# Kernel optimization log

Hardware: AMD Instinct MI355X
Metric: run time of the kernel (lower is better)

Reference implementation:

```python
import jax, jax.numpy as jnp
import numpy as np

HIDDEN = 1024
HEADS = 16
HEAD_DIM = HIDDEN // HEADS
B, T = 4, 2048


def setup_inputs() -> dict:
    key = jax.random.key(0)
    k_x, k_w1, k_b1, k_w2, k_b2 = jax.random.split(key, 5)
    lim1 = 1.0 / np.sqrt(HIDDEN)
    x = jax.random.normal(k_x, (B, T, HIDDEN), dtype=jnp.float32)
    # causal lower-triangular mask, broadcastable to [B, H, T, T]
    mask = jnp.tril(jnp.ones((T, T), dtype=jnp.int32))[None, None, :, :]
    # qkv_proj: Linear(HIDDEN, 3*HIDDEN); torch Linear: y = x @ W.T + b
    W_qkv = jax.random.uniform(k_w1, (3 * HIDDEN, HIDDEN), minval=-lim1, maxval=lim1, dtype=jnp.float32)
    b_qkv = jax.random.uniform(k_b1, (3 * HIDDEN,), minval=-lim1, maxval=lim1, dtype=jnp.float32)
    W_out = jax.random.uniform(k_w2, (HIDDEN, HIDDEN), minval=-lim1, maxval=lim1, dtype=jnp.float32)
    b_out = jax.random.uniform(k_b2, (HIDDEN,), minval=-lim1, maxval=lim1, dtype=jnp.float32)
    return {"x": x, "mask": mask, "W_qkv": W_qkv, "b_qkv": b_qkv, "W_out": W_out, "b_out": b_out}


def reference(x, mask, W_qkv, b_qkv, W_out, b_out):
    Bx, Tx, C = x.shape
    qkv = x @ W_qkv.T + b_qkv                      # [B, T, 3C]
    qkv = qkv.reshape(Bx, Tx, 3, HEADS, HEAD_DIM)
    qkv = jnp.transpose(qkv, (2, 0, 3, 1, 4))      # [3, B, H, T, Dh]
    Q, K, V = qkv[0], qkv[1], qkv[2]
    scale = 1.0 / np.sqrt(HEAD_DIM)
    scores = jnp.einsum('bhqd,bhkd->bhqk', Q, K) * scale  # [B, H, T, T]
    scores = jnp.where(mask == 0, -jnp.inf, scores)
    probs = jax.nn.softmax(scores, axis=-1)
    ctx = jnp.einsum('bhqk,bhkd->bhqd', probs, V)  # [B, H, T, Dh]
    ctx = jnp.transpose(ctx, (0, 2, 1, 3)).reshape(Bx, Tx, C)
    return ctx @ W_out.T + b_out
```

## Files before the change

### kernel.cpp

```cpp
#include <hip/hip_runtime.h>
#include <cstdint>
#include <cstddef>

#define B_ 4
#define T_ 2048
#define C_ 1024
#define H_ 16
#define D_ 64

typedef __attribute__((ext_vector_type(8))) __bf16 bf16x8;
typedef __attribute__((ext_vector_type(4))) float floatx4;

#define QSCL (0.125f * 1.44269504088896f)
#define FMAX 24.0f

__device__ __forceinline__ unsigned short f2bf(float f) {
  union { float f; unsigned int u; } v; v.f = f;
  unsigned int r = v.u + 0x7fffu + ((v.u >> 16) & 1u);
  return (unsigned short)(r >> 16);
}
__device__ __forceinline__ ushort4 pk4(float a, float b, float c, float d) {
  ushort4 u; u.x = f2bf(a); u.y = f2bf(b); u.z = f2bf(c); u.w = f2bf(d);
  return u;
}
__device__ __forceinline__ bf16x8 cvt8(float4 a, float4 b) {
  bf16x8 r;
  r[0] = a.x; r[1] = a.y; r[2] = a.z; r[3] = a.w;
  r[4] = b.x; r[5] = b.y; r[6] = b.z; r[7] = b.w;
  return r;
}
__device__ __forceinline__ ushort4 pk4c(float a, float b, float c, float d) {
  union { __bf16 b4[4]; ushort4 u; } w;
  w.b4[0] = (__bf16)a; w.b4[1] = (__bf16)b; w.b4[2] = (__bf16)c; w.b4[3] = (__bf16)d;
  return w.u;
}

__device__ __forceinline__ void gl_lds16(const void* g, void* l) {
  __builtin_amdgcn_global_load_lds(
      (const __attribute__((address_space(1))) unsigned int*)g,
      (__attribute__((address_space(3))) unsigned int*)l, 16, 0, 0);
}

__global__ __launch_bounds__(256)
void conv_bf16(const float* __restrict__ src, unsigned short* __restrict__ dst,
               int n8) {
  for (int i = blockIdx.x * 256 + threadIdx.x; i < n8; i += gridDim.x * 256) {
    const float4* s = (const float4*)src + 2 * (size_t)i;
    float4 a = s[0], b = s[1];
    ((bf16x8*)dst)[i] = cvt8(a, b);
  }
}

template<int EPI, int GATHER, int WBF>
__global__ __launch_bounds__(256, 3)
void gemm_bt(const unsigned short* __restrict__ Abf,
             const void* __restrict__ Wraw,
             const float* __restrict__ bias,
             float* __restrict__ out,
             unsigned short* __restrict__ qws,
             unsigned short* __restrict__ kws,
             unsigned short* __restrict__ vtws)
{
  alignas(16) __shared__ unsigned short As[128 * 64];
  alignas(16) __shared__ unsigned short Bs[WBF ? 128 * 64 : 128 * 72];
  const int tid  = threadIdx.x;
  const int lane = tid & 63;
  const int wid  = tid >> 6;
  const int col  = lane & 15;
  const int quad = lane >> 4;
  const int wm = (wid >> 1) << 6;
  const int wn = (wid & 1) << 6;
  const int bm = blockIdx.y << 7;
  const int bn = blockIdx.x << 7;

  const float* Wf          = (const float*)Wraw;
  const unsigned short* Wb = (const unsigned short*)Wraw;

  const int r0 = tid >> 3;
  const int c0 = tid & 7;

  floatx4 acc[4][4];
#pragma unroll
  for (int i = 0; i < 4; ++i)
#pragma unroll
    for (int j = 0; j < 4; ++j)
      acc[i][j] = (floatx4){0.f, 0.f, 0.f, 0.f};

  for (int k0 = 0; k0 < 1024; k0 += 64) {
    __syncthreads();
#pragma unroll
    for (int s = 0; s < 4; ++s) {
      const int row  = (s << 5) + r0;
      const int colE = ((c0 ^ (row & 7)) << 3);
      const unsigned short* gsrc;
      if (GATHER) {
        const int m = bm + row;
        const int b = m >> 11, t = m & 2047;
        const int h = k0 >> 6;
        gsrc = Abf + ((((size_t)(b * 16 + h) << 11) + t) << 6) + colE;
      } else {
        gsrc = Abf + (size_t)(bm + row) * 1024 + k0 + colE;
      }
      gl_lds16(gsrc, (char*)As + (s << 12) + (wid << 10));
    }
    if (WBF) {
#pragma unroll
      for (int s = 0; s < 4; ++s) {
        const int row  = (s << 5) + r0;
        const int colE = ((c0 ^ (row & 7)) << 3);
        const unsigned short* gsrc = Wb + (size_t)(bn + row) * 1024 + k0 + colE;
        gl_lds16(gsrc, (char*)Bs + (s << 12) + (wid << 10));
      }
    } else {
#pragma unroll
      for (int s = 0; s < 4; ++s) {
        const int row = (s << 5) + r0;
        const int kc  = c0 << 3;
        const float* wsrc = &Wf[(size_t)(bn + row) * 1024 + k0 + kc];
        float4 w0 = *(const float4*)wsrc;
        float4 w1 = *(const float4*)(wsrc + 4);
        *(bf16x8*)&Bs[row * 72 + kc] = cvt8(w0, w1);
      }
    }
    __syncthreads();
#pragma unroll
    for (int kk = 0; kk < 64; kk += 32) {
      bf16x8 af[4], bfr[4];
#pragma unroll
      for (int i = 0; i < 4; ++i) {
        const int r = wm + i * 16 + col;
        af[i] = *(const bf16x8*)&As[(r << 6) + ((kk + quad * 8) ^ ((r & 7) << 3))];
      }
#pragma unroll
      for (int j = 0; j < 4; ++j) {
        const int r = wn + j * 16 + col;
        if (WBF)
          bfr[j] = *(const bf16x8*)&Bs[(r << 6) + ((kk + quad * 8) ^ ((r & 7) << 3))];
        else
          bfr[j] = *(const bf16x8*)&Bs[r * 72 + kk + quad * 8];
      }
#pragma unroll
      for (int i = 0; i < 4; ++i)
#pragma unroll
        for (int j = 0; j < 4; ++j)
          acc[i][j] = __builtin_amdgcn_mfma_f32_16x16x32_bf16(af[i], bfr[j], acc[i][j], 0, 0, 0);
    }
  }

#pragma unroll
  for (int i = 0; i < 4; ++i) {
    const int row = bm + wm + i * 16 + quad * 4;
#pragma unroll
    for (int j = 0; j < 4; ++j) {
      const int n  = bn + wn + j * 16 + col;
      const float bv = bias[n];
      float v[4];
#pragma unroll
      for (int r = 0; r < 4; ++r) v[r] = acc[i][j][r] + bv;

      if (EPI == 1) {
#pragma unroll
        for (int r = 0; r < 4; ++r)
          out[(size_t)(row + r) * 1024 + n] = v[r];
      } else {
        const int s   = n >> 10;
        const int rem = n & 1023;
        const int h   = rem >> 6;
        const int d   = rem & 63;
        const int b   = row >> 11;
        const int t   = row & 2047;
        const size_t bh = (size_t)(b * H_ + h);
        if (s == 0) {
#pragma unroll
          for (int r = 0; r < 4; ++r)
            qws[(bh * T_ + t + r) * D_ + d] = f2bf(v[r] * QSCL);
        } else if (s == 1) {
#pragma unroll
          for (int r = 0; r < 4; ++r)
            kws[(bh * T_ + t + r) * D_ + d] = f2bf(v[r]);
        } else {
          *(ushort4*)&vtws[(bh * D_ + d) * T_ + t] = pk4(v[0], v[1], v[2], v[3]);
        }
      }
    }
  }
}

__global__ __launch_bounds__(256, 2)
void attn_causal(unsigned short* __restrict__ qws,
                 const unsigned short* __restrict__ kws,
                 const unsigned short* __restrict__ vtws)
{
  alignas(16) __shared__ unsigned short Ks[2][64 * 64];
  alignas(16) __shared__ unsigned short Vs[2][64 * 64];
  alignas(16) __shared__ unsigned short Ps[4][2][16][72];
  const int tid  = threadIdx.x;
  const int lane = tid & 63;
  const int wid  = tid >> 6;
  const int col  = lane & 15;
  const int quad = lane >> 4;

  const int bh = blockIdx.x & 63;
  const int pr = blockIdx.x >> 6;

  const unsigned short* Kp  = kws + (size_t)bh * T_ * D_;
  const unsigned short* Vtp = vtws + (size_t)bh * D_ * T_;

  const int srow8 = lane >> 3;
  const int swz   = ((lane & 7) ^ srow8) << 3;

#define STAGE(kt_, b_)                                                        \
  do {                                                                        \
    _Pragma("unroll") for (int c2 = 0; c2 < 2; ++c2) {                        \
      const int cb = wid + (c2 << 2);                   \
      gl_lds16(Kp + ((size_t)(((kt_) << 6) + (cb << 3) + srow8) << 6) + swz,  \
               (char*)&Ks[b_][0] + (cb << 10));                               \
      gl_lds16(Vtp + ((size_t)((cb << 3) + srow8) << 11) + ((kt_) << 6) + swz,\
               (char*)&Vs[b_][0] + (cb << 10));                               \
    }                                                                         \
  } while (0)

#pragma unroll
  for (int half = 0; half < 2; ++half) {
    const int band = (half == 0) ? pr : (15 - pr);
    const int nk   = (band << 1) + 2;
    const int q0   = (band << 7) + (wid << 5);
    unsigned short* Qp = qws + ((size_t)bh * T_ + q0) * D_;

    bf16x8 bq[2][2];
#pragma unroll
    for (int h = 0; h < 2; ++h) {
      bq[h][0] = *(const bf16x8*)&Qp[(h * 16 + col) * D_ + quad * 8];
      bq[h][1] = *(const bf16x8*)&Qp[(h * 16 + col) * D_ + 32 + quad * 8];
    }

    floatx4 o[2][4];
#pragma unroll
    for (int h = 0; h < 2; ++h)
#pragma unroll
      for (int j = 0; j < 4; ++j) o[h][j] = (floatx4){0.f, 0.f, 0.f, 0.f};
    float lrow[2] = {0.f, 0.f};

    STAGE(0, 0);
    __syncthreads();

    for (int kt = 0; kt < nk; ++kt) {
      const int buf = kt & 1;
      if (kt + 1 < nk) STAGE(kt + 1, buf ^ 1);

      const unsigned short* Kb = &Ks[buf][0];
      bf16x8 kA[4], kB[4];
#pragma unroll
      for (int g = 0; g < 4; ++g) {
        const int r = g * 16 + col;
        kA[g] = *(const bf16x8*)&Kb[(r << 6) + ((quad ^ (col & 7)) << 3)];
        kB[g] = *(const bf16x8*)&Kb[(r << 6) + (((quad | 4) ^ (col & 7)) << 3)];
      }

      floatx4 s[2][4];
#pragma unroll
      for (int h = 0; h < 2; ++h)
#pragma unroll
        for (int g = 0; g < 4; ++g) {
          s[h][g] = (floatx4){0.f, 0.f, 0.f, 0.f};
          s[h][g] = __builtin_amdgcn_mfma_f32_16x16x32_bf16(kA[g], bq[h][0], s[h][g], 0, 0, 0);
          s[h][g] = __builtin_amdgcn_mfma_f32_16x16x32_bf16(kB[g], bq[h][1], s[h][g], 0, 0, 0);
        }

      if (kt >= nk - 2) {
#pragma unroll
        for (int h = 0; h < 2; ++h) {
          const int lim = q0 - (kt << 6) + (h << 4) + col;
#pragma unroll
          for (int g = 0; g < 4; ++g)
#pragma unroll
            for (int r = 0; r < 4; ++r)
              if (g * 16 + quad * 4 + r > lim) s[h][g][r] = -1e30f;
        }
      }

#pragma unroll
      for (int h = 0; h < 2; ++h) {
#pragma unroll
        for (int g = 0; g < 4; ++g)
#pragma unroll
          for (int r = 0; r < 4; ++r)
            s[h][g][r] = exp2f(s[h][g][r] - FMAX);
        lrow[h] += ((s[h][0][0] + s[h][0][1]) + (s[h][0][2] + s[h][0][3])) +
                   ((s[h][1][0] + s[h][1][1]) + (s[h][1][2] + s[h][1][3])) +
                   ((s[h][2][0] + s[h][2][1]) + (s[h][2][2] + s[h][2][3])) +
                   ((s[h][3][0] + s[h][3][1]) + (s[h][3][2] + s[h][3][3]));
      }

#pragma unroll
      for (int h = 0; h < 2; ++h)
#pragma unroll
        for (int g = 0; g < 4; ++g)
          *(ushort4*)&Ps[wid][h][col][g * 16 + quad * 4] =
              pk4c(s[h][g][0], s[h][g][1], s[h][g][2], s[h][g][3]);
      asm volatile("s_waitcnt lgkmcnt(0)" ::: "memory");

      const unsigned short* Vb = &Vs[buf][0];
      bf16x8 vA[4], vB[4];
#pragma unroll
      for (int j = 0; j < 4; ++j) {
        const int r = j * 16 + col;
        vA[j] = *(const bf16x8*)&Vb[(r << 6) + ((quad ^ (col & 7)) << 3)];
        vB[j] = *(const bf16x8*)&Vb[(r << 6) + (((quad | 4) ^ (col & 7)) << 3)];
      }

#pragma unroll
      for (int h = 0; h < 2; ++h) {
        const bf16x8 ap0 = *(const bf16x8*)&Ps[wid][h][col][quad * 8];
        const bf16x8 ap1 = *(const bf16x8*)&Ps[wid][h][col][32 + quad * 8];
#pragma unroll
        for (int j = 0; j < 4; ++j) {
          o[h][j] = __builtin_amdgcn_mfma_f32_16x16x32_bf16(ap0, vA[j], o[h][j], 0, 0, 0);
          o[h][j] = __builtin_amdgcn_mfma_f32_16x16x32_bf16(ap1, vB[j], o[h][j], 0, 0, 0);
        }
      }

      __syncthreads();
    }

#pragma unroll
    for (int h = 0; h < 2; ++h) {
      lrow[h] += __shfl_xor(lrow[h], 16);
      lrow[h] += __shfl_xor(lrow[h], 32);
      float lr[4];
#pragma unroll
      for (int r = 0; r < 4; ++r) lr[r] = 1.0f / __shfl(lrow[h], quad * 4 + r);
#pragma unroll
      for (int j = 0; j < 4; ++j)
#pragma unroll
        for (int r = 0; r < 4; ++r)
          Qp[(size_t)(h * 16 + quad * 4 + r) * D_ + j * 16 + col] =
              f2bf(o[h][j][r] * lr[r]);
    }
  }
#undef STAGE
}

extern "C" void kernel_launch(void* const* d_in, const int* in_sizes, int n_in,
                              void* d_out, int out_size, void* d_ws, size_t ws_size,
                              hipStream_t stream) {
  const float* x     = (const float*)d_in[0];
  const float* W_qkv = (const float*)d_in[2];
  const float* b_qkv = (const float*)d_in[3];
  const float* W_out = (const float*)d_in[4];
  const float* b_out = (const float*)d_in[5];
  float* out = (float*)d_out;

  const size_t per = (size_t)B_ * H_ * T_ * D_;
  unsigned short* qws  = (unsigned short*)d_ws;
  unsigned short* vtws = qws + per;
  unsigned short* kws  = (unsigned short*)d_out;
  unsigned short* xbf  = kws + per;

  const bool bigws = ws_size >= (size_t)38 * 1024 * 1024;
  unsigned short* wqbf = vtws + per;

  conv_bf16<<<dim3(2048), 256, 0, stream>>>(x, xbf, (int)(per >> 3));

  if (bigws) {
    conv_bf16<<<dim3(768), 256, 0, stream>>>(W_qkv, wqbf, (3 * C_ * C_) >> 3);
    gemm_bt<0, 0, 1><<<dim3(3072 / 128, 8192 / 128), 256, 0, stream>>>(
        xbf, (const void*)wqbf, b_qkv, nullptr, qws, kws, vtws);
  } else {
    gemm_bt<0, 0, 0><<<dim3(3072 / 128, 8192 / 128), 256, 0, stream>>>(
        xbf, (const void*)W_qkv, b_qkv, nullptr, qws, kws, vtws);
  }

  attn_causal<<<dim3(8 * 64), 256, 0, stream>>>(qws, kws, vtws);

  conv_bf16<<<dim3(512), 256, 0, stream>>>(W_out, vtws, (C_ * C_) >> 3);

  gemm_bt<1, 1, 1><<<dim3(1024 / 128, 8192 / 128), 256, 0, stream>>>(
      qws, (const void*)vtws, b_out, out, nullptr, nullptr, nullptr);
}
```

Baseline: 270.3 us.

## Fuse input conversions, compute softmax row sums via MFMA, add setprio hints

Merges the x and W_qkv fp32-to-bf16 conversions into one launch to save a kernel launch. In the attention kernel, the -FMAX offset moves into the MFMA accumulator initialiser, and the per-row sum of probabilities is computed by extra MFMAs against a vector of ones instead of scalar adds and cross-lane shuffles. The MFMA sections are wrapped in s_setprio raises. Costs are two extra MFMAs per tile, and the row sums are now taken from the bf16-rounded probabilities.

Result: faster. 263.4 us (-2.5%).

```diff
diff --git a/kernel.cpp b/kernel.cpp
--- a/kernel.cpp
+++ b/kernel.cpp
@@ -48,6 +48,18 @@
     const float4* s = (const float4*)src + 2 * (size_t)i;
     float4 a = s[0], b = s[1];
     ((bf16x8*)dst)[i] = cvt8(a, b);
+  }
+}
+
+__global__ __launch_bounds__(256)
+void conv_dual(const float* __restrict__ s1, unsigned short* __restrict__ d1, int n1,
+               const float* __restrict__ s2, unsigned short* __restrict__ d2, int n2) {
+  for (int i = blockIdx.x * 256 + threadIdx.x; i < n1 + n2; i += gridDim.x * 256) {
+    const float4* sp; bf16x8* dp;
+    if (i < n1) { sp = (const float4*)s1 + 2 * (size_t)i;       dp = (bf16x8*)d1 + i; }
+    else { int j = i - n1; sp = (const float4*)s2 + 2 * (size_t)j; dp = (bf16x8*)d2 + j; }
+    float4 a = sp[0], b = sp[1];
+    *dp = cvt8(a, b);
   }
 }
 
@@ -206,6 +218,10 @@
   const unsigned short* Kp  = kws + (size_t)bh * T_ * D_;
   const unsigned short* Vtp = vtws + (size_t)bh * D_ * T_;
 
+  bf16x8 vones;
+#pragma unroll
+  for (int i = 0; i < 8; ++i) vones[i] = (__bf16)1.0f;
+
   const int srow8 = lane >> 3;
   const int swz   = ((lane & 7) ^ srow8) << 3;
 
@@ -234,12 +250,13 @@
       bq[h][1] = *(const bf16x8*)&Qp[(h * 16 + col) * D_ + 32 + quad * 8];
     }
 
-    floatx4 o[2][4];
-#pragma unroll
-    for (int h = 0; h < 2; ++h)
+    floatx4 o[2][4], ol[2];
+#pragma unroll
+    for (int h = 0; h < 2; ++h) {
+      ol[h] = (floatx4){0.f, 0.f, 0.f, 0.f};
 #pragma unroll
       for (int j = 0; j < 4; ++j) o[h][j] = (floatx4){0.f, 0.f, 0.f, 0.f};
-    float lrow[2] = {0.f, 0.f};
+    }
 
     STAGE(0, 0);
     __syncthreads();
@@ -258,14 +275,16 @@
       }
 
       floatx4 s[2][4];
+      __builtin_amdgcn_s_setprio(1);
 #pragma unroll
       for (int h = 0; h < 2; ++h)
 #pragma unroll
         for (int g = 0; g < 4; ++g) {
-          s[h][g] = (floatx4){0.f, 0.f, 0.f, 0.f};
+          s[h][g] = (floatx4){-FMAX, -FMAX, -FMAX, -FMAX};
           s[h][g] = __builtin_amdgcn_mfma_f32_16x16x32_bf16(kA[g], bq[h][0], s[h][g], 0, 0, 0);
           s[h][g] = __builtin_amdgcn_mfma_f32_16x16x32_bf16(kB[g], bq[h][1], s[h][g], 0, 0, 0);
         }
+      __builtin_amdgcn_s_setprio(0);
 
       if (kt >= nk - 2) {
 #pragma unroll
@@ -280,17 +299,12 @@
       }
 
 #pragma unroll
-      for (int h = 0; h < 2; ++h) {
+      for (int h = 0; h < 2; ++h)
 #pragma unroll
         for (int g = 0; g < 4; ++g)
 #pragma unroll
           for (int r = 0; r < 4; ++r)
-            s[h][g][r] = exp2f(s[h][g][r] - FMAX);
-        lrow[h] += ((s[h][0][0] + s[h][0][1]) + (s[h][0][2] + s[h][0][3])) +
-                   ((s[h][1][0] + s[h][1][1]) + (s[h][1][2] + s[h][1][3])) +
-                   ((s[h][2][0] + s[h][2][1]) + (s[h][2][2] + s[h][2][3])) +
-                   ((s[h][3][0] + s[h][3][1]) + (s[h][3][2] + s[h][3][3]));
-      }
+            s[h][g][r] = exp2f(s[h][g][r]);
 
 #pragma unroll
       for (int h = 0; h < 2; ++h)
@@ -309,6 +323,7 @@
         vB[j] = *(const bf16x8*)&Vb[(r << 6) + (((quad | 4) ^ (col & 7)) << 3)];
       }
 
+      __builtin_amdgcn_s_setprio(1);
 #pragma unroll
       for (int h = 0; h < 2; ++h) {
         const bf16x8 ap0 = *(const bf16x8*)&Ps[wid][h][col][quad * 8];
@@ -318,18 +333,19 @@
           o[h][j] = __builtin_amdgcn_mfma_f32_16x16x32_bf16(ap0, vA[j], o[h][j], 0, 0, 0);
           o[h][j] = __builtin_amdgcn_mfma_f32_16x16x32_bf16(ap1, vB[j], o[h][j], 0, 0, 0);
         }
-      }
+        ol[h] = __builtin_amdgcn_mfma_f32_16x16x32_bf16(ap0, vones, ol[h], 0, 0, 0);
+        ol[h] = __builtin_amdgcn_mfma_f32_16x16x32_bf16(ap1, vones, ol[h], 0, 0, 0);
+      }
+      __builtin_amdgcn_s_setprio(0);
 
       __syncthreads();
     }
 
 #pragma unroll
     for (int h = 0; h < 2; ++h) {
-      lrow[h] += __shfl_xor(lrow[h], 16);
-      lrow[h] += __shfl_xor(lrow[h], 32);
       float lr[4];
 #pragma unroll
-      for (int r = 0; r < 4; ++r) lr[r] = 1.0f / __shfl(lrow[h], quad * 4 + r);
+      for (int r = 0; r < 4; ++r) lr[r] = 1.0f / ol[h][r];
 #pragma unroll
       for (int j = 0; j < 4; ++j)
 #pragma unroll
@@ -360,13 +376,13 @@
   const bool bigws = ws_size >= (size_t)38 * 1024 * 1024;
   unsigned short* wqbf = vtws + per;
 
-  conv_bf16<<<dim3(2048), 256, 0, stream>>>(x, xbf, (int)(per >> 3));
-
   if (bigws) {
-    conv_bf16<<<dim3(768), 256, 0, stream>>>(W_qkv, wqbf, (3 * C_ * C_) >> 3);
+    conv_dual<<<dim3(2048), 256, 0, stream>>>(x, xbf, (int)(per >> 3),
+                                              W_qkv, wqbf, (3 * C_ * C_) >> 3);
     gemm_bt<0, 0, 1><<<dim3(3072 / 128, 8192 / 128), 256, 0, stream>>>(
         xbf, (const void*)wqbf, b_qkv, nullptr, qws, kws, vtws);
   } else {
+    conv_bf16<<<dim3(2048), 256, 0, stream>>>(x, xbf, (int)(per >> 3));
     gemm_bt<0, 0, 0><<<dim3(3072 / 128, 8192 / 128), 256, 0, stream>>>(
         xbf, (const void*)W_qkv, b_qkv, nullptr, qws, kws, vtws);
   }
```
